# Optimization experiments

Measured on AMD Instinct MI355X. Metric: run time of the kernel, lower is better.

The kernel has to match this reference:

```python
import jax, jax.numpy as jnp
import numpy as np

N_NODES = 50000
N_EDGES = 600000
D = 128
HEADS = 4
CH = D // HEADS  # 32 channels per head
NEG_SLOPE = 0.2


def setup_inputs() -> dict:
    key = jax.random.key(0)
    ks = jax.random.split(key, 16)
    x = jax.random.normal(ks[0], (N_NODES, D), dtype=jnp.float32)
    # edges with src != dst so that appending self-loops matches PyG's
    # remove_self_loops + add_self_loops exactly
    src = jax.random.randint(ks[1], (N_EDGES,), 0, N_NODES, dtype=jnp.int32)
    off = jax.random.randint(ks[2], (N_EDGES,), 1, N_NODES, dtype=jnp.int32)
    dst = (src + off) % N_NODES
    edge_index = jnp.stack([src, dst], axis=0)
    s = 1.0 / np.sqrt(D)
    def layer_params(k):
        k1, k2, k3, k4 = jax.random.split(k, 4)
        return (jax.random.normal(k1, (D, D), jnp.float32) * s,
                jax.random.normal(k2, (HEADS, CH), jnp.float32) * s,
                jax.random.normal(k3, (HEADS, CH), jnp.float32) * s,
                jnp.zeros((D,), jnp.float32),
                jax.random.normal(k4, (D, D), jnp.float32) * s)
    W1, att_src1, att_dst1, bias1, Wskip1 = layer_params(ks[3])
    W2, att_src2, att_dst2, bias2, Wskip2 = layer_params(ks[4])
    return dict(x=x, edge_index=edge_index,
                W1=W1, att_src1=att_src1, att_dst1=att_dst1, bias1=bias1, Wskip1=Wskip1,
                W2=W2, att_src2=att_src2, att_dst2=att_dst2, bias2=bias2, Wskip2=Wskip2)


def _gat_block(x, src, dst, W, a_src, a_dst, bias, Wskip):
    N = x.shape[0]
    h = (x @ W).reshape(N, HEADS, CH)                       # [N,H,C]
    asrc = jnp.einsum('nhc,hc->nh', h, a_src)               # [N,H]
    adst = jnp.einsum('nhc,hc->nh', h, a_dst)
    e = jax.nn.leaky_relu(asrc[src] + adst[dst], NEG_SLOPE)  # [E,H]
    m = jax.ops.segment_max(e, dst, num_segments=N)
    m = jnp.where(jnp.isfinite(m), m, 0.0)                  # guard empty segments
    e = jnp.exp(e - m[dst])
    denom = jax.ops.segment_sum(e, dst, num_segments=N)
    alpha = e / (denom[dst] + 1e-16)                        # segment softmax over dst
    msg = h[src] * alpha[:, :, None]                        # [E,H,C]
    agg = jax.ops.segment_sum(msg, dst, num_segments=N)
    out = agg.reshape(N, D) + bias + x @ Wskip              # conv + skip
    return jax.nn.elu(out)


def reference(x, edge_index, W1, att_src1, att_dst1, bias1, Wskip1,
              W2, att_src2, att_dst2, bias2, Wskip2):
    N = x.shape[0]
    loops = jnp.arange(N, dtype=edge_index.dtype)
    src = jnp.concatenate([edge_index[0], loops])
    dst = jnp.concatenate([edge_index[1], loops])
    x = _gat_block(x, src, dst, W1, att_src1, att_dst1, bias1, Wskip1)
    x = _gat_block(x, src, dst, W2, att_src2, att_dst2, bias2, Wskip2)
    return x
```

## Files before the change

kernel.cpp:

```cpp
#include <hip/hip_runtime.h>
#include <hip/hip_bf16.h>

#define NN 50000
#define NE 600000
#define DD 128
#define NH 4
#define ET (NE + NN)
#define NEG_SLOPE 0.2f
#define NB 196

typedef __attribute__((ext_vector_type(8))) short short8;
typedef __attribute__((ext_vector_type(4))) float f32x4;

__device__ __forceinline__ float bf2f(unsigned short u) {
    union { unsigned int i; float f; } c; c.i = ((unsigned int)u) << 16; return c.f;
}
__device__ __forceinline__ unsigned short f2bf(float f) {
    union { float f; unsigned int i; } c; c.f = f;
    unsigned int r = c.i + 0x7FFF + ((c.i >> 16) & 1);
    return (unsigned short)(r >> 16);
}


__global__ void __launch_bounds__(256) prep_k(const float* __restrict__ W1, const float* __restrict__ Ws1,
                                              const float* __restrict__ W2, const float* __restrict__ Ws2,
                                              unsigned short* __restrict__ Wt, int* __restrict__ counts) {
    int idx = blockIdx.x * 256 + threadIdx.x;
    int mat = idx >> 14;
    int p = idx & 16383;
    int col = p >> 7;
    int cs = (p >> 3) & 15;
    int j = p & 7;
    int c = cs ^ (col & 7);
    int k = c * 8 + j;
    const float* Wsrc = (mat == 0) ? W1 : (mat == 1) ? Ws1 : (mat == 2) ? W2 : Ws2;
    Wt[idx] = f2bf(Wsrc[k * DD + col]);
    if (idx < NN) counts[idx] = 1;
}

__global__ void __launch_bounds__(256) count_k(const int* __restrict__ dst, int* __restrict__ counts) {
    int e = blockIdx.x * 256 + threadIdx.x;
    if (e < NE) atomicAdd(&counts[dst[e]], 1);
}


__global__ void __launch_bounds__(256) partial_k(const int* __restrict__ counts, int* __restrict__ bsum) {
    __shared__ int tmp[256];
    int t = blockIdx.x * 256 + threadIdx.x;
    int v = (t < NN) ? counts[t] : 0;
    tmp[threadIdx.x] = v;
    __syncthreads();
    for (int off = 128; off > 0; off >>= 1) {
        if (threadIdx.x < off) tmp[threadIdx.x] += tmp[threadIdx.x + off];
        __syncthreads();
    }
    if (threadIdx.x == 0) bsum[blockIdx.x] = tmp[0];
}

__global__ void __launch_bounds__(256) scanb_k(const int* __restrict__ bsum, int* __restrict__ boff) {
    __shared__ int tmp[256];
    int tid = threadIdx.x;
    int v = (tid < NB) ? bsum[tid] : 0;
    tmp[tid] = v;
    __syncthreads();
    for (int off = 1; off < 256; off <<= 1) {
        int u = (tid >= off) ? tmp[tid - off] : 0;
        __syncthreads();
        tmp[tid] += u;
        __syncthreads();
    }
    if (tid < NB) boff[tid] = tmp[tid] - v;
}

__global__ void __launch_bounds__(256) offsets_k(const int* __restrict__ counts, const int* __restrict__ boff,
                                                 int* __restrict__ offsets, int* __restrict__ cursor,
                                                 int* __restrict__ esrc) {
    __shared__ int tmp[256];
    int b = blockIdx.x, tid = threadIdx.x;
    int t = b * 256 + tid;
    int v = (t < NN) ? counts[t] : 0;
    tmp[tid] = v;
    __syncthreads();
    for (int off = 1; off < 256; off <<= 1) {
        int u = (tid >= off) ? tmp[tid - off] : 0;
        __syncthreads();
        tmp[tid] += u;
        __syncthreads();
    }
    if (t < NN) {
        int o = boff[b] + tmp[tid] - v;
        offsets[t] = o;
        cursor[t] = o;
        esrc[o + v - 1] = t;
    }
    if (b == 0 && tid == 0) offsets[NN] = ET;
}

__global__ void __launch_bounds__(256) scatter_k(const int* __restrict__ src, const int* __restrict__ dst,
                                                 int* __restrict__ cursor, int* __restrict__ esrc) {
    int e = blockIdx.x * 256 + threadIdx.x;
    if (e < NE) {
        int pos = atomicAdd(&cursor[dst[e]], 1);
        esrc[pos] = src[e];
    }
}


template <bool F32IN>
__global__ void __launch_bounds__(256) gemm2_k(const void* __restrict__ xin,
                                               const unsigned short* __restrict__ Wl,
                                               const float* __restrict__ a_src, const float* __restrict__ a_dst,
                                               unsigned short* __restrict__ h2, unsigned short* __restrict__ skipb,
                                               float* __restrict__ nsrc, float* __restrict__ ndst) {
    __shared__ __align__(16) unsigned char wlds[65536];
    int row0 = blockIdx.x * 64;
    int tid = threadIdx.x;

    int w = tid >> 6, lidx = tid & 63;
    int lrow = lidx & 15, lk = lidx >> 4;
    int srow = row0 + w * 16 + lrow;
    int rclamp = srow < NN ? srow : NN - 1;

    short8 afrag[4];
    if (F32IN) {
        const float* xp = (const float*)xin + (size_t)rclamp * DD;
#pragma unroll
        for (int kc = 0; kc < 4; ++kc) {
            float4 u0 = *(const float4*)(xp + kc * 32 + lk * 8);
            float4 u1 = *(const float4*)(xp + kc * 32 + lk * 8 + 4);
            short8 a;
            a[0] = (short)f2bf(u0.x); a[1] = (short)f2bf(u0.y);
            a[2] = (short)f2bf(u0.z); a[3] = (short)f2bf(u0.w);
            a[4] = (short)f2bf(u1.x); a[5] = (short)f2bf(u1.y);
            a[6] = (short)f2bf(u1.z); a[7] = (short)f2bf(u1.w);
            afrag[kc] = a;
        }
    } else {
        const unsigned short* xp = (const unsigned short*)xin + (size_t)rclamp * DD;
#pragma unroll
        for (int kc = 0; kc < 4; ++kc)
            afrag[kc] = *(const short8*)(xp + kc * 32 + lk * 8);
    }

    {
        const uint4* g = (const uint4*)Wl;
        uint4* l = (uint4*)wlds;
#pragma unroll
        for (int i = 0; i < 16; ++i)
            l[i * 256 + tid] = g[i * 256 + tid];
    }
    __syncthreads();

    f32x4 zero = {0.f, 0.f, 0.f, 0.f};
    f32x4 acch[8], accs[8];
#pragma unroll
    for (int t = 0; t < 8; ++t) { acch[t] = zero; accs[t] = zero; }

#pragma unroll
    for (int kc = 0; kc < 4; ++kc) {
        short8 a = afrag[kc];
#pragma unroll
        for (int t = 0; t < 8; ++t) {
            int off = (t * 16 + lrow) * 256 + (((kc * 4 + lk) ^ (lrow & 7)) * 16);
            short8 b  = *(const short8*)&wlds[off];
            short8 bs = *(const short8*)&wlds[off + 32768];
            acch[t] = __builtin_amdgcn_mfma_f32_16x16x32_bf16(a, b, acch[t], 0, 0, 0);
            accs[t] = __builtin_amdgcn_mfma_f32_16x16x32_bf16(a, bs, accs[t], 0, 0, 0);
        }
    }

#pragma unroll
    for (int t = 0; t < 8; ++t) {
#pragma unroll
        for (int q = 0; q < 4; ++q) {
            int grow = row0 + w * 16 + lk * 4 + q;
            if (grow < NN) {
                int col = t * 16 + lrow;
                h2[(size_t)grow * DD + col] = f2bf(acch[t][q]);
                skipb[(size_t)grow * DD + col] = f2bf(accs[t][q]);
            }
        }
    }

    float as_lo[NH], as_hi[NH], ad_lo[NH], ad_hi[NH];
#pragma unroll
    for (int h = 0; h < NH; ++h) {
        as_lo[h] = a_src[h * 32 + lrow];
        as_hi[h] = a_src[h * 32 + 16 + lrow];
        ad_lo[h] = a_dst[h * 32 + lrow];
        ad_hi[h] = a_dst[h * 32 + 16 + lrow];
    }
#pragma unroll
    for (int h = 0; h < NH; ++h) {
#pragma unroll
        for (int q = 0; q < 4; ++q) {
            float ps = acch[2 * h][q] * as_lo[h] + acch[2 * h + 1][q] * as_hi[h];
            float pd = acch[2 * h][q] * ad_lo[h] + acch[2 * h + 1][q] * ad_hi[h];
#pragma unroll
            for (int off = 1; off < 16; off <<= 1) {
                ps += __shfl_xor(ps, off);
                pd += __shfl_xor(pd, off);
            }
            if (lrow == 0) {
                int grow = row0 + w * 16 + lk * 4 + q;
                if (grow < NN) {
                    nsrc[grow * 4 + h] = ps;
                    ndst[grow * 4 + h] = pd;
                }
            }
        }
    }
}


__global__ void __launch_bounds__(256) aggregate_k(const unsigned short* __restrict__ h2,
                                                   const unsigned short* __restrict__ skipb,
                                                   const float* __restrict__ nsrc, const float* __restrict__ ndst,
                                                   const int* __restrict__ offsets, const int* __restrict__ esrc,
                                                   const float* __restrict__ bias, float* __restrict__ outf,
                                                   unsigned short* __restrict__ outb) {
    int n = blockIdx.x * 4 + (threadIdx.x >> 6);
    int i = threadIdx.x & 63;
    int e = i & 15, hc = i >> 4;
    int gbase = i & 48;
    int beg = offsets[n], end = offsets[n + 1];
    float ad = ndst[n * 4 + hc];
    const unsigned int* h2w = (const unsigned int*)h2;

    float m = -1e30f, den = 0.f, acc0 = 0.f, acc1 = 0.f;
    for (int base = beg; base < end; base += 16) {
        int j = base + e;
        int jc = j < end ? j : end - 1;
        int s = esrc[jc];
        float a = nsrc[s * 4 + hc] + ad;
        a = a > 0.f ? a : NEG_SLOPE * a;
        if (j >= end) a = -1e30f;
        float cm = a;
        cm = fmaxf(cm, __shfl_xor(cm, 1));
        cm = fmaxf(cm, __shfl_xor(cm, 2));
        cm = fmaxf(cm, __shfl_xor(cm, 4));
        cm = fmaxf(cm, __shfl_xor(cm, 8));
        float mn = fmaxf(m, cm);
        float scale = __expf(m - mn);
        float wgt = __expf(a - mn);
        m = mn;
        float sw = wgt;
        sw += __shfl_xor(sw, 1);
        sw += __shfl_xor(sw, 2);
        sw += __shfl_xor(sw, 4);
        sw += __shfl_xor(sw, 8);
        den = den * scale + sw;
        acc0 *= scale;
        acc1 *= scale;
#pragma unroll
        for (int e2 = 0; e2 < 16; ++e2) {
            int se = __shfl(s, e2);
            float we = __shfl(wgt, gbase + e2);
            unsigned hv = h2w[se * 64 + i];
            acc0 = fmaf(we, bf2f((unsigned short)(hv & 0xFFFF)), acc0);
            acc1 = fmaf(we, bf2f((unsigned short)(hv >> 16)), acc1);
        }
    }
    float inv = 1.f / (den + 1e-16f);
    int c0 = 2 * i;
    unsigned sk = ((const unsigned int*)skipb)[n * 64 + i];
    float2 bv = *(const float2*)&bias[c0];
    float o0 = acc0 * inv + bv.x + bf2f((unsigned short)(sk & 0xFFFF));
    float o1 = acc1 * inv + bv.y + bf2f((unsigned short)(sk >> 16));
    o0 = o0 > 0.f ? o0 : expm1f(o0);
    o1 = o1 > 0.f ? o1 : expm1f(o1);
    size_t o = (size_t)n * DD;
    if (outf) { outf[o + c0] = o0; outf[o + c0 + 1] = o1; }
    if (outb) { outb[o + c0] = f2bf(o0); outb[o + c0 + 1] = f2bf(o1); }
}


extern "C" void kernel_launch(void* const* d_in, const int* in_sizes, int n_in,
                              void* d_out, int out_size, void* d_ws, size_t ws_size,
                              hipStream_t stream) {
    const float* x   = (const float*)d_in[0];
    const int* eidx  = (const int*)d_in[1];
    const float* W1  = (const float*)d_in[2];
    const float* as1 = (const float*)d_in[3];
    const float* ad1 = (const float*)d_in[4];
    const float* b1  = (const float*)d_in[5];
    const float* Ws1 = (const float*)d_in[6];
    const float* W2  = (const float*)d_in[7];
    const float* as2 = (const float*)d_in[8];
    const float* ad2 = (const float*)d_in[9];
    const float* b2  = (const float*)d_in[10];
    const float* Ws2 = (const float*)d_in[11];
    float* out = (float*)d_out;

    const int* e_src = eidx;
    const int* e_dst = eidx + NE;

    char* p = (char*)d_ws;
    unsigned short* h2    = (unsigned short*)p; p += (size_t)NN * DD * 2;
    unsigned short* xb    = (unsigned short*)p; p += (size_t)NN * DD * 2;
    unsigned short* skipb = (unsigned short*)p; p += (size_t)NN * DD * 2;
    float* nsrc = (float*)p; p += (size_t)NN * NH * 4;
    float* ndst = (float*)p; p += (size_t)NN * NH * 4;
    unsigned short* Wt = (unsigned short*)p; p += (size_t)4 * DD * DD * 2;
    int* counts  = (int*)p; p += (size_t)NN * 4;
    int* offsets = (int*)p; p += (size_t)(NN + 1) * 4;
    int* cursor  = (int*)p; p += (size_t)NN * 4;
    int* bsum    = (int*)p; p += 256 * 4;
    int* boff    = (int*)p; p += 256 * 4;
    int* esrc    = (int*)p; p += (size_t)ET * 4;

    prep_k<<<256, 256, 0, stream>>>(W1, Ws1, W2, Ws2, Wt, counts);
    count_k<<<(NE + 255) / 256, 256, 0, stream>>>(e_dst, counts);
    partial_k<<<NB, 256, 0, stream>>>(counts, bsum);
    scanb_k<<<1, 256, 0, stream>>>(bsum, boff);
    offsets_k<<<NB, 256, 0, stream>>>(counts, boff, offsets, cursor, esrc);
    scatter_k<<<(NE + 255) / 256, 256, 0, stream>>>(e_src, e_dst, cursor, esrc);

    const int GG = (NN + 63) / 64;

    gemm2_k<true><<<GG, 256, 0, stream>>>(x, Wt, as1, ad1, h2, skipb, nsrc, ndst);
    aggregate_k<<<NN / 4, 256, 0, stream>>>(h2, skipb, nsrc, ndst, offsets, esrc, b1, nullptr, xb);

    gemm2_k<false><<<GG, 256, 0, stream>>>(xb, Wt + 32768, as2, ad2, h2, skipb, nsrc, ndst);
    aggregate_k<<<NN / 4, 256, 0, stream>>>(h2, skipb, nsrc, ndst, offsets, esrc, b2, out, nullptr);
}
```

Baseline: 268.9 us.

## Fuse edge counting into first GEMM and replace multi-kernel scan with single-block scan

Replaces the three-kernel prefix sum (partial, block scan, offsets) with one 1024-thread single-block scan that reads counts as int4 and adds the self-loop count inline. The edge-degree counting atomics become extra blocks appended to the first GEMM launch, so the two run in the same grid. The GEMM blocks are enlarged to 512 threads covering 128 rows, which halves the per-row cost of loading weights into LDS. This removes several kernel launches and serialisation points, but a single-block scan over 50k nodes may be slow, and the atomic blocks now share the GPU with GEMM blocks.

```diff
diff --git a/kernel.cpp b/kernel.cpp
--- a/kernel.cpp
+++ b/kernel.cpp
@@ -7,7 +7,6 @@
 #define NH 4
 #define ET (NE + NN)
 #define NEG_SLOPE 0.2f
-#define NB 196
 
 typedef __attribute__((ext_vector_type(8))) short short8;
 typedef __attribute__((ext_vector_type(4))) float f32x4;
@@ -35,65 +34,50 @@
     int k = c * 8 + j;
     const float* Wsrc = (mat == 0) ? W1 : (mat == 1) ? Ws1 : (mat == 2) ? W2 : Ws2;
     Wt[idx] = f2bf(Wsrc[k * DD + col]);
-    if (idx < NN) counts[idx] = 1;
-}
-
-__global__ void __launch_bounds__(256) count_k(const int* __restrict__ dst, int* __restrict__ counts) {
-    int e = blockIdx.x * 256 + threadIdx.x;
-    if (e < NE) atomicAdd(&counts[dst[e]], 1);
-}
-
-
-__global__ void __launch_bounds__(256) partial_k(const int* __restrict__ counts, int* __restrict__ bsum) {
-    __shared__ int tmp[256];
-    int t = blockIdx.x * 256 + threadIdx.x;
-    int v = (t < NN) ? counts[t] : 0;
-    tmp[threadIdx.x] = v;
+    if (idx < NN) counts[idx] = 0;
+}
+
+
+__global__ void __launch_bounds__(1024) scan_k(const int* __restrict__ counts, int* __restrict__ offsets,
+                                               int* __restrict__ cursor, int* __restrict__ esrc) {
+    __shared__ int part[1024];
+    int tid = threadIdx.x;
+    const int4* c4 = (const int4*)counts;
+    const int NI4 = NN / 4;
+    const int CH = (NI4 + 1023) / 1024;
+    int beg4 = tid * CH;
+    int end4 = beg4 + CH < NI4 ? beg4 + CH : NI4;
+    int s = 0;
+    for (int i = beg4; i < end4; ++i) {
+        int4 v = c4[i];
+        s += v.x + v.y + v.z + v.w + 4;
+    }
+    part[tid] = s;
     __syncthreads();
-    for (int off = 128; off > 0; off >>= 1) {
-        if (threadIdx.x < off) tmp[threadIdx.x] += tmp[threadIdx.x + off];
+    for (int off = 1; off < 1024; off <<= 1) {
+        int v = (tid >= off) ? part[tid - off] : 0;
         __syncthreads();
-    }
-    if (threadIdx.x == 0) bsum[blockIdx.x] = tmp[0];
-}
-
-__global__ void __launch_bounds__(256) scanb_k(const int* __restrict__ bsum, int* __restrict__ boff) {
-    __shared__ int tmp[256];
-    int tid = threadIdx.x;
-    int v = (tid < NB) ? bsum[tid] : 0;
-    tmp[tid] = v;
-    __syncthreads();
-    for (int off = 1; off < 256; off <<= 1) {
-        int u = (tid >= off) ? tmp[tid - off] : 0;
+        part[tid] += v;
         __syncthreads();
-        tmp[tid] += u;
-        __syncthreads();
-    }
-    if (tid < NB) boff[tid] = tmp[tid] - v;
-}
-
-__global__ void __launch_bounds__(256) offsets_k(const int* __restrict__ counts, const int* __restrict__ boff,
-                                                 int* __restrict__ offsets, int* __restrict__ cursor,
-                                                 int* __restrict__ esrc) {
-    __shared__ int tmp[256];
-    int b = blockIdx.x, tid = threadIdx.x;
-    int t = b * 256 + tid;
-    int v = (t < NN) ? counts[t] : 0;
-    tmp[tid] = v;
-    __syncthreads();
-    for (int off = 1; off < 256; off <<= 1) {
-        int u = (tid >= off) ? tmp[tid - off] : 0;
-        __syncthreads();
-        tmp[tid] += u;
-        __syncthreads();
-    }
-    if (t < NN) {
-        int o = boff[b] + tmp[tid] - v;
-        offsets[t] = o;
-        cursor[t] = o;
-        esrc[o + v - 1] = t;
-    }
-    if (b == 0 && tid == 0) offsets[NN] = ET;
+    }
+    int running = part[tid] - s;
+    for (int i = beg4; i < end4; ++i) {
+        int4 v = c4[i];
+        int node = i * 4;
+        int4 o;
+        o.x = running;
+        o.y = o.x + v.x + 1;
+        o.z = o.y + v.y + 1;
+        o.w = o.z + v.z + 1;
+        running = o.w + v.w + 1;
+        ((int4*)offsets)[i] = o;
+        ((int4*)cursor)[i] = o;
+        esrc[o.x + v.x] = node;
+        esrc[o.y + v.y] = node + 1;
+        esrc[o.z + v.z] = node + 2;
+        esrc[o.w + v.w] = node + 3;
+    }
+    if (tid == 0) offsets[NN] = ET;
 }
 
 __global__ void __launch_bounds__(256) scatter_k(const int* __restrict__ src, const int* __restrict__ dst,
@@ -106,16 +90,23 @@
 }
 
 
+#define GGEMM ((NN + 127) / 128)
+
 template <bool F32IN>
-__global__ void __launch_bounds__(256) gemm2_k(const void* __restrict__ xin,
+__global__ void __launch_bounds__(512) gemm2_k(const void* __restrict__ xin,
                                                const unsigned short* __restrict__ Wl,
                                                const float* __restrict__ a_src, const float* __restrict__ a_dst,
                                                unsigned short* __restrict__ h2, unsigned short* __restrict__ skipb,
-                                               float* __restrict__ nsrc, float* __restrict__ ndst) {
+                                               float* __restrict__ nsrc, float* __restrict__ ndst,
+                                               const int* __restrict__ e_dst, int* __restrict__ counts) {
     __shared__ __align__(16) unsigned char wlds[65536];
-    int row0 = blockIdx.x * 64;
+    if (F32IN && blockIdx.x >= GGEMM) {
+        int e = (blockIdx.x - GGEMM) * 512 + threadIdx.x;
+        if (e < NE) atomicAdd(&counts[e_dst[e]], 1);
+        return;
+    }
+    int row0 = blockIdx.x * 128;
     int tid = threadIdx.x;
-
     int w = tid >> 6, lidx = tid & 63;
     int lrow = lidx & 15, lk = lidx >> 4;
     int srow = row0 + w * 16 + lrow;
@@ -146,8 +137,8 @@
         const uint4* g = (const uint4*)Wl;
         uint4* l = (uint4*)wlds;
 #pragma unroll
-        for (int i = 0; i < 16; ++i)
-            l[i * 256 + tid] = g[i * 256 + tid];
+        for (int i = 0; i < 8; ++i)
+            l[i * 512 + tid] = g[i * 512 + tid];
     }
     __syncthreads();
 
@@ -303,24 +294,21 @@
     float* ndst = (float*)p; p += (size_t)NN * NH * 4;
     unsigned short* Wt = (unsigned short*)p; p += (size_t)4 * DD * DD * 2;
     int* counts  = (int*)p; p += (size_t)NN * 4;
-    int* offsets = (int*)p; p += (size_t)(NN + 1) * 4;
+    int* offsets = (int*)p; p += (size_t)(NN + 4) * 4;
     int* cursor  = (int*)p; p += (size_t)NN * 4;
-    int* bsum    = (int*)p; p += 256 * 4;
-    int* boff    = (int*)p; p += 256 * 4;
     int* esrc    = (int*)p; p += (size_t)ET * 4;
 
+    const int CB = (NE + 511) / 512;
+
     prep_k<<<256, 256, 0, stream>>>(W1, Ws1, W2, Ws2, Wt, counts);
-    count_k<<<(NE + 255) / 256, 256, 0, stream>>>(e_dst, counts);
-    partial_k<<<NB, 256, 0, stream>>>(counts, bsum);
-    scanb_k<<<1, 256, 0, stream>>>(bsum, boff);
-    offsets_k<<<NB, 256, 0, stream>>>(counts, boff, offsets, cursor, esrc);
+
+    gemm2_k<true><<<GGEMM + CB, 512, 0, stream>>>(x, Wt, as1, ad1, h2, skipb, nsrc, ndst, e_dst, counts);
+
+    scan_k<<<1, 1024, 0, stream>>>(counts, offsets, cursor, esrc);
     scatter_k<<<(NE + 255) / 256, 256, 0, stream>>>(e_src, e_dst, cursor, esrc);
 
-    const int GG = (NN + 63) / 64;
-
-    gemm2_k<true><<<GG, 256, 0, stream>>>(x, Wt, as1, ad1, h2, skipb, nsrc, ndst);
     aggregate_k<<<NN / 4, 256, 0, stream>>>(h2, skipb, nsrc, ndst, offsets, esrc, b1, nullptr, xb);
 
-    gemm2_k<false><<<GG, 256, 0, stream>>>(xb, Wt + 32768, as2, ad2, h2, skipb, nsrc, ndst);
+    gemm2_k<false><<<GGEMM, 512, 0, stream>>>(xb, Wt + 32768, as2, ad2, h2, skipb, nsrc, ndst, e_dst, counts);
     aggregate_k<<<NN / 4, 256, 0, stream>>>(h2, skipb, nsrc, ndst, offsets, esrc, b2, out, nullptr);
 }
```

Measured after the change: 300.5 us. +11.8%, slower.

## Fold edge counting into first GEMM launch and merge scan kernels

Applied to the files above, without the earlier changes.

Removes the separate count kernel by appending extra blocks to the first GEMM launch that do the dst-degree atomics. The self-loop +1 is now added at read time instead of by initialization. The block-sum scan is merged into offsets_k, where every block redundantly scans the block sums. The GEMM block grows to 512 threads covering 128 rows, which halves the weight LDS loads per row but doubles the threads sharing one block. Together this cuts launches from 10 to 8, at the cost of redundant scan work and possible contention between the atomic blocks and the GEMM blocks.

```diff
diff --git a/kernel.cpp b/kernel.cpp
--- a/kernel.cpp
+++ b/kernel.cpp
@@ -35,19 +35,14 @@
     int k = c * 8 + j;
     const float* Wsrc = (mat == 0) ? W1 : (mat == 1) ? Ws1 : (mat == 2) ? W2 : Ws2;
     Wt[idx] = f2bf(Wsrc[k * DD + col]);
-    if (idx < NN) counts[idx] = 1;
-}
-
-__global__ void __launch_bounds__(256) count_k(const int* __restrict__ dst, int* __restrict__ counts) {
-    int e = blockIdx.x * 256 + threadIdx.x;
-    if (e < NE) atomicAdd(&counts[dst[e]], 1);
+    if (idx < NN) counts[idx] = 0;
 }
 
 
 __global__ void __launch_bounds__(256) partial_k(const int* __restrict__ counts, int* __restrict__ bsum) {
     __shared__ int tmp[256];
     int t = blockIdx.x * 256 + threadIdx.x;
-    int v = (t < NN) ? counts[t] : 0;
+    int v = (t < NN) ? counts[t] + 1 : 0;
     tmp[threadIdx.x] = v;
     __syncthreads();
     for (int off = 128; off > 0; off >>= 1) {
@@ -57,10 +52,26 @@
     if (threadIdx.x == 0) bsum[blockIdx.x] = tmp[0];
 }
 
-__global__ void __launch_bounds__(256) scanb_k(const int* __restrict__ bsum, int* __restrict__ boff) {
+__global__ void __launch_bounds__(256) offsets_k(const int* __restrict__ counts, const int* __restrict__ bsum,
+                                                 int* __restrict__ offsets, int* __restrict__ cursor,
+                                                 int* __restrict__ esrc) {
+    __shared__ int bs[256];
     __shared__ int tmp[256];
-    int tid = threadIdx.x;
-    int v = (tid < NB) ? bsum[tid] : 0;
+    int b = blockIdx.x, tid = threadIdx.x;
+    int bv = (tid < NB) ? bsum[tid] : 0;
+    bs[tid] = bv;
+    __syncthreads();
+    for (int off = 1; off < 256; off <<= 1) {
+        int u = (tid >= off) ? bs[tid - off] : 0;
+        __syncthreads();
+        bs[tid] += u;
+        __syncthreads();
+    }
+    int boff = (b == 0) ? 0 : bs[b - 1];
+
+    int t = b * 256 + tid;
+    int c = (t < NN) ? counts[t] : 0;
+    int v = (t < NN) ? c + 1 : 0;
     tmp[tid] = v;
     __syncthreads();
     for (int off = 1; off < 256; off <<= 1) {
@@ -69,29 +80,11 @@
         tmp[tid] += u;
         __syncthreads();
     }
-    if (tid < NB) boff[tid] = tmp[tid] - v;
-}
-
-__global__ void __launch_bounds__(256) offsets_k(const int* __restrict__ counts, const int* __restrict__ boff,
-                                                 int* __restrict__ offsets, int* __restrict__ cursor,
-                                                 int* __restrict__ esrc) {
-    __shared__ int tmp[256];
-    int b = blockIdx.x, tid = threadIdx.x;
-    int t = b * 256 + tid;
-    int v = (t < NN) ? counts[t] : 0;
-    tmp[tid] = v;
-    __syncthreads();
-    for (int off = 1; off < 256; off <<= 1) {
-        int u = (tid >= off) ? tmp[tid - off] : 0;
-        __syncthreads();
-        tmp[tid] += u;
-        __syncthreads();
-    }
     if (t < NN) {
-        int o = boff[b] + tmp[tid] - v;
+        int o = boff + tmp[tid] - v;
         offsets[t] = o;
         cursor[t] = o;
-        esrc[o + v - 1] = t;
+        esrc[o + c] = t;
     }
     if (b == 0 && tid == 0) offsets[NN] = ET;
 }
@@ -106,16 +99,23 @@
 }
 
 
+#define GGEMM ((NN + 127) / 128)
+
 template <bool F32IN>
-__global__ void __launch_bounds__(256) gemm2_k(const void* __restrict__ xin,
+__global__ void __launch_bounds__(512) gemm2_k(const void* __restrict__ xin,
                                                const unsigned short* __restrict__ Wl,
                                                const float* __restrict__ a_src, const float* __restrict__ a_dst,
                                                unsigned short* __restrict__ h2, unsigned short* __restrict__ skipb,
-                                               float* __restrict__ nsrc, float* __restrict__ ndst) {
+                                               float* __restrict__ nsrc, float* __restrict__ ndst,
+                                               const int* __restrict__ e_dst, int* __restrict__ counts) {
     __shared__ __align__(16) unsigned char wlds[65536];
-    int row0 = blockIdx.x * 64;
+    if (F32IN && blockIdx.x >= GGEMM) {
+        int e = (blockIdx.x - GGEMM) * 512 + threadIdx.x;
+        if (e < NE) atomicAdd(&counts[e_dst[e]], 1);
+        return;
+    }
+    int row0 = blockIdx.x * 128;
     int tid = threadIdx.x;
-
     int w = tid >> 6, lidx = tid & 63;
     int lrow = lidx & 15, lk = lidx >> 4;
     int srow = row0 + w * 16 + lrow;
@@ -146,8 +146,8 @@
         const uint4* g = (const uint4*)Wl;
         uint4* l = (uint4*)wlds;
 #pragma unroll
-        for (int i = 0; i < 16; ++i)
-            l[i * 256 + tid] = g[i * 256 + tid];
+        for (int i = 0; i < 8; ++i)
+            l[i * 512 + tid] = g[i * 512 + tid];
     }
     __syncthreads();
 
@@ -303,24 +303,23 @@
     float* ndst = (float*)p; p += (size_t)NN * NH * 4;
     unsigned short* Wt = (unsigned short*)p; p += (size_t)4 * DD * DD * 2;
     int* counts  = (int*)p; p += (size_t)NN * 4;
-    int* offsets = (int*)p; p += (size_t)(NN + 1) * 4;
+    int* offsets = (int*)p; p += (size_t)(NN + 4) * 4;
     int* cursor  = (int*)p; p += (size_t)NN * 4;
     int* bsum    = (int*)p; p += 256 * 4;
-    int* boff    = (int*)p; p += 256 * 4;
     int* esrc    = (int*)p; p += (size_t)ET * 4;
 
+    const int CB = (NE + 511) / 512;
+
     prep_k<<<256, 256, 0, stream>>>(W1, Ws1, W2, Ws2, Wt, counts);
-    count_k<<<(NE + 255) / 256, 256, 0, stream>>>(e_dst, counts);
+
+    gemm2_k<true><<<GGEMM + CB, 512, 0, stream>>>(x, Wt, as1, ad1, h2, skipb, nsrc, ndst, e_dst, counts);
+
     partial_k<<<NB, 256, 0, stream>>>(counts, bsum);
-    scanb_k<<<1, 256, 0, stream>>>(bsum, boff);
-    offsets_k<<<NB, 256, 0, stream>>>(counts, boff, offsets, cursor, esrc);
+    offsets_k<<<NB, 256, 0, stream>>>(counts, bsum, offsets, cursor, esrc);
     scatter_k<<<(NE + 255) / 256, 256, 0, stream>>>(e_src, e_dst, cursor, esrc);
 
-    const int GG = (NN + 63) / 64;
-
-    gemm2_k<true><<<GG, 256, 0, stream>>>(x, Wt, as1, ad1, h2, skipb, nsrc, ndst);
     aggregate_k<<<NN / 4, 256, 0, stream>>>(h2, skipb, nsrc, ndst, offsets, esrc, b1, nullptr, xb);
 
-    gemm2_k<false><<<GG, 256, 0, stream>>>(xb, Wt + 32768, as2, ad2, h2, skipb, nsrc, ndst);
+    gemm2_k<false><<<GGEMM, 512, 0, stream>>>(xb, Wt + 32768, as2, ad2, h2, skipb, nsrc, ndst, e_dst, counts);
     aggregate_k<<<NN / 4, 256, 0, stream>>>(h2, skipb, nsrc, ndst, offsets, esrc, b2, out, nullptr);
 }
```

Result: faster. 250.0 us (median of 2 runs) (-7.0%).
